# Kernel tuning notes

Measured on AMD Instinct MI355X. Metric: run time of the kernel, lower is better.

Reference implementation:

```python
import jax, jax.numpy as jnp
import numpy as np

N_NODES = 50000
N_EDGES = 600000
CH = 128


def _mlp(h, w1, b1, w2, b2):
    # Linear -> ReLU -> Linear (weights stored [in, out])
    return jax.nn.relu(h @ w1 + b1) @ w2 + b2


def setup_inputs() -> dict:
    key = jax.random.key(0)
    ks = jax.random.split(key, 12)
    def lin(k, fan_in, fan_out):
        bound = 1.0 / np.sqrt(fan_in)
        kw, kb = jax.random.split(k)
        w = jax.random.uniform(kw, (fan_in, fan_out), jnp.float32, -bound, bound)
        b = jax.random.uniform(kb, (fan_out,), jnp.float32, -bound, bound)
        return w, b
    ew1, eb1 = lin(ks[0], 3 * CH, CH)
    ew2, eb2 = lin(ks[1], CH, CH)
    nw1, nb1 = lin(ks[2], 2 * CH, CH)
    nw2, nb2 = lin(ks[3], CH, CH)
    x = jax.random.normal(ks[4], (N_NODES, CH), jnp.float32)
    edge_attr = jax.random.normal(ks[5], (N_EDGES, CH), jnp.float32)
    edge_index = jax.random.randint(ks[6], (2, N_EDGES), 0, N_NODES, jnp.int64 if jax.config.read('jax_enable_x64') else jnp.int32)
    return {"x": x, "edge_index": edge_index, "edge_attr": edge_attr,
            "ew1": ew1, "eb1": eb1, "ew2": ew2, "eb2": eb2,
            "nw1": nw1, "nb1": nb1, "nw2": nw2, "nb2": nb2}


def reference(x, edge_index, edge_attr, ew1, eb1, ew2, eb2, nw1, nb1, nw2, nb2):
    row, col = edge_index[0], edge_index[1]
    n = x.shape[0]
    # edge model: concat(source, target, edge_attr) -> MLP -> new edge_attr
    e_in = jnp.concatenate([x[row], x[col], edge_attr], axis=1)  # [E, 3*ch]
    new_edge_attr = _mlp(e_in, ew1, eb1, ew2, eb2)               # [E, ch]
    # node model: concat(x[col], new_edge_attr) -> MLP -> scatter_mean over row
    n_in = jnp.concatenate([x[col], new_edge_attr], axis=1)      # [E, 2*ch]
    msg = _mlp(n_in, nw1, nb1, nw2, nb2)                         # [E, ch]
    seg_sum = jax.ops.segment_sum(msg, row, num_segments=n)      # [N, ch]
    cnt = jax.ops.segment_sum(jnp.ones((msg.shape[0],), msg.dtype), row, num_segments=n)
    new_x = seg_sum / jnp.maximum(cnt, 1.0)[:, None]             # scatter_mean
    return new_x, new_edge_attr
```

## Files before the change

### kernel.cpp

```cpp
#include <hip/hip_runtime.h>
#include <stdint.h>

#define NN 50000
#define NE 600000
#define CH 128
#define RT 2
#define EPB 128

typedef __attribute__((ext_vector_type(8))) short short8;
typedef __attribute__((ext_vector_type(4))) float f32x4;
typedef __attribute__((ext_vector_type(4))) uint32_t u32x4;

__device__ __forceinline__ ushort f2bf(float f) {
  union { float f; uint32_t u; } v; v.f = f;
  uint32_t u = v.u;
  return (ushort)((u + 0x7FFFu + ((u >> 16) & 1u)) >> 16);
}
__device__ __forceinline__ float bf2f(uint32_t u16) {
  union { uint32_t u; float f; } t; t.u = u16 << 16; return t.f;
}
__device__ __forceinline__ uint32_t cvtpk_bf16(float a, float b) {
  uint32_t r;
  asm("v_cvt_pk_bf16_f32 %0, %1, %2" : "=v"(r) : "v"(a), "v"(b));
  return r;
}

__global__ void prep_frag_k(const float* __restrict__ ew1, const float* __restrict__ ew2,
                            const float* __restrict__ nw1, const float* __restrict__ nw2,
                            ushort* __restrict__ wB) {
  int idx = blockIdx.x * 256 + threadIdx.x;
  if (idx >= 114688) return;
  const float* src; int local;
  if (idx < 49152)      { src = ew1; local = idx; }
  else if (idx < 65536) { src = ew2; local = idx - 49152; }
  else if (idx < 98304) { src = nw1; local = idx - 65536; }
  else                  { src = nw2; local = idx - 98304; }
  int ks   = local >> 12;
  int rem  = local & 4095;
  int nt   = rem >> 9;
  int t    = rem & 511;
  int lane = t >> 3, i = t & 7;
  int k = ks * 32 + (lane >> 4) * 8 + i;
  int n = nt * 16 + (lane & 15);
  wB[idx] = f2bf(src[k * 128 + n]);
}

__global__ void convert_x_k(const float* __restrict__ x, ushort* __restrict__ xb) {
  int i = blockIdx.x * 256 + threadIdx.x;
  if (i >= NN * CH / 4) return;
  const float4 f = reinterpret_cast<const float4*>(x)[i];
  ushort4 r;
  r.x = f2bf(f.x); r.y = f2bf(f.y); r.z = f2bf(f.z); r.w = f2bf(f.w);
  reinterpret_cast<ushort4*>(xb)[i] = r;
}

__global__ void rank_k(const int* __restrict__ ei, unsigned* __restrict__ cnt,
                       unsigned* __restrict__ rank) {
  int e = blockIdx.x * 256 + threadIdx.x;
  if (e < NE) rank[e] = atomicAdd(&cnt[ei[e]], 1u);
}

__global__ void scan_k(const unsigned* __restrict__ cnt, unsigned* __restrict__ start) {
  __shared__ unsigned s[1024];
  const int CHUNK = (NN + 1023) / 1024;
  int t = threadIdx.x;
  int lo = t * CHUNK, hi = lo + CHUNK < NN ? lo + CHUNK : NN;
  unsigned sum = 0;
  for (int i = lo; i < hi; ++i) sum += cnt[i];
  s[t] = sum;
  __syncthreads();
  for (int off = 1; off < 1024; off <<= 1) {
    unsigned v = (t >= off) ? s[t - off] : 0u;
    __syncthreads();
    s[t] += v;
    __syncthreads();
  }
  unsigned run = t ? s[t - 1] : 0u;
  for (int i = lo; i < hi; ++i) { start[i] = run; run += cnt[i]; }
}

__global__ void dest_k(const int* __restrict__ ei, const unsigned* __restrict__ start,
                       const unsigned* __restrict__ rank, unsigned* __restrict__ dest) {
  int e = blockIdx.x * 256 + threadIdx.x;
  if (e < NE) dest[e] = start[ei[e]] + rank[e];
}

__device__ __forceinline__ void mm8(const ushort* Bcbuf, int lane,
                                    const short8 a[RT], f32x4 acc[RT][8]) {
#pragma unroll
  for (int nt = 0; nt < 8; ++nt) {
    short8 b = *reinterpret_cast<const short8*>(Bcbuf + nt * 512 + lane * 8);
#pragma unroll
    for (int rt = 0; rt < RT; ++rt)
      acc[rt][nt] = __builtin_amdgcn_mfma_f32_16x16x32_bf16(a[rt], b, acc[rt][nt], 0, 0, 0);
  }
}

__global__ __launch_bounds__(256, 2) void fused_k(
    const int* __restrict__ ei, const float* __restrict__ edge_attr,
    const ushort* __restrict__ wB,
    const float* __restrict__ eb1, const float* __restrict__ eb2,
    const float* __restrict__ nb1, const float* __restrict__ nb2,
    const ushort* __restrict__ xb, const unsigned* __restrict__ dest,
    ushort* __restrict__ msg, float* __restrict__ out_e)
{
  __shared__ ushort hbuf[4][RT * 16][136];
  __shared__ ushort Bc[4][4096];
  const int tid  = threadIdx.x;
  const int lane = tid & 63;
  const int widx = tid >> 6;
  const int wbase = blockIdx.x * EPB + widx * (RT * 16);
  const int l15 = lane & 15;
  const int g = lane >> 4;
  const int kg = g * 8;
  ushort (*h)[136] = hbuf[widx];

  short8 bt[2][4];

#define LDB2(set, ph) do { \
    const ushort* _s = wB + (size_t)(ph) * 4096 + tid * 16; \
    bt[set][0] = *reinterpret_cast<const short8*>(_s); \
    bt[set][1] = *reinterpret_cast<const short8*>(_s + 8); \
    bt[set][2] = *reinterpret_cast<const short8*>(_s + 4096); \
    bt[set][3] = *reinterpret_cast<const short8*>(_s + 4096 + 8); \
  } while (0)
#define STB2(set, ph) do { \
    ushort* _d0 = &Bc[(ph) & 3][tid * 16]; \
    ushort* _d1 = &Bc[((ph) + 1) & 3][tid * 16]; \
    *reinterpret_cast<short8*>(_d0)     = bt[set][0]; \
    *reinterpret_cast<short8*>(_d0 + 8) = bt[set][1]; \
    *reinterpret_cast<short8*>(_d1)     = bt[set][2]; \
    *reinterpret_cast<short8*>(_d1 + 8) = bt[set][3]; \
  } while (0)
#define BAR() do { \
    asm volatile("s_waitcnt lgkmcnt(0)" ::: "memory"); \
    __builtin_amdgcn_s_barrier(); \
  } while (0)
#define STEP(s, A0, A1, DO_LDB, DO_STB, DO_BAR) do { \
    __builtin_amdgcn_s_setprio(1); \
    mm8(Bc[(2 * (s)) & 3], lane, A0, acc); \
    mm8(Bc[(2 * (s) + 1) & 3], lane, A1, acc); \
    __builtin_amdgcn_s_setprio(0); \
    if (DO_LDB) LDB2((s) & 1, 2 * (s) + 4); \
    if (DO_STB) STB2(((s) + 1) & 1, 2 * (s) + 2); \
    if (DO_BAR) BAR(); \
  } while (0)
#define LDH(dst, ksl) do { \
    _Pragma("unroll") \
    for (int _rt = 0; _rt < RT; ++_rt) \
      dst[_rt] = *reinterpret_cast<const short8*>(&h[_rt * 16 + l15][(ksl) * 32 + kg]); \
  } while (0)

  LDB2(0, 0);
  LDB2(1, 2);

  int rowA[RT], colA[RT], eAc[RT];
#pragma unroll
  for (int rt = 0; rt < RT; ++rt) {
    int e = wbase + rt * 16 + l15;
    eAc[rt] = e < NE ? e : NE - 1;
    rowA[rt] = ei[eAc[rt]];
    colA[rt] = ei[NE + eAc[rt]];
  }
  short8 axr[4][RT], axc[4][RT];
#pragma unroll
  for (int ksl = 0; ksl < 4; ++ksl)
#pragma unroll
    for (int rt = 0; rt < RT; ++rt) {
      axr[ksl][rt] = *reinterpret_cast<const short8*>(xb + rowA[rt] * CH + ksl * 32 + kg);
      axc[ksl][rt] = *reinterpret_cast<const short8*>(xb + colA[rt] * CH + ksl * 32 + kg);
    }
  short8 eab[4][RT];
#pragma unroll
  for (int ksl = 0; ksl < 4; ++ksl)
#pragma unroll
    for (int rt = 0; rt < RT; ++rt) {
      const float* pp = edge_attr + (size_t)eAc[rt] * CH + ksl * 32 + kg;
      float4 f0 = *reinterpret_cast<const float4*>(pp);
      float4 f1 = *reinterpret_cast<const float4*>(pp + 4);
      union { u32x4 u; short8 s; } cv;
      cv.u = (u32x4){ cvtpk_bf16(f0.x, f0.y), cvtpk_bf16(f0.z, f0.w),
                      cvtpk_bf16(f1.x, f1.y), cvtpk_bf16(f1.z, f1.w) };
      eab[ksl][rt] = cv.s;
    }
  unsigned dp[RT * 4];
#pragma unroll
  for (int it = 0; it < RT * 4; ++it) {
    int er = wbase + it * 4 + g;
    dp[it] = dest[er < NE ? er : NE - 1];
  }

  STB2(0, 0);
  BAR();

  const f32x4 zero4 = {0.f, 0.f, 0.f, 0.f};
  f32x4 acc[RT][8];
  short8 ha0[RT], ha1[RT];

#pragma unroll
  for (int rt = 0; rt < RT; ++rt)
#pragma unroll
    for (int nt = 0; nt < 8; ++nt) acc[rt][nt] = zero4;

  STEP(0, axr[0], axr[1], 1, 1, 1);
  STEP(1, axr[2], axr[3], 1, 1, 1);
  STEP(2, axc[0], axc[1], 1, 1, 1);
  STEP(3, axc[2], axc[3], 1, 1, 1);
  STEP(4, eab[0], eab[1], 1, 1, 1);
  STEP(5, eab[2], eab[3], 1, 1, 1);
#pragma unroll
  for (int nt = 0; nt < 8; ++nt) {
    float bb = eb1[nt * 16 + l15];
#pragma unroll
    for (int rt = 0; rt < RT; ++rt)
#pragma unroll
      for (int r = 0; r < 4; r += 2) {
        float v0 = fmaxf(acc[rt][nt][r] + bb, 0.f);
        float v1 = fmaxf(acc[rt][nt][r + 1] + bb, 0.f);
        uint32_t pk = cvtpk_bf16(v0, v1);
        h[rt * 16 + g * 4 + r][nt * 16 + l15]     = (ushort)(pk & 0xffffu);
        h[rt * 16 + g * 4 + r + 1][nt * 16 + l15] = (ushort)(pk >> 16);
      }
  }

#pragma unroll
  for (int rt = 0; rt < RT; ++rt)
#pragma unroll
    for (int nt = 0; nt < 8; ++nt) acc[rt][nt] = zero4;
  LDH(ha0, 0); LDH(ha1, 1);
  STEP(6, ha0, ha1, 1, 1, 1);
  LDH(ha0, 2); LDH(ha1, 3);
  STEP(7, ha0, ha1, 1, 1, 1);
#pragma unroll
  for (int nt = 0; nt < 8; ++nt) {
    float bb = eb2[nt * 16 + l15];
#pragma unroll
    for (int rt = 0; rt < RT; ++rt) {
      float v[4];
#pragma unroll
      for (int r = 0; r < 4; ++r) {
        v[r] = acc[rt][nt][r] + bb;
        int erow = wbase + rt * 16 + g * 4 + r;
        if (erow < NE) out_e[(size_t)erow * CH + nt * 16 + l15] = v[r];
      }
#pragma unroll
      for (int r = 0; r < 4; r += 2) {
        uint32_t pk = cvtpk_bf16(v[r], v[r + 1]);
        h[rt * 16 + g * 4 + r][nt * 16 + l15]     = (ushort)(pk & 0xffffu);
        h[rt * 16 + g * 4 + r + 1][nt * 16 + l15] = (ushort)(pk >> 16);
      }
    }
  }

#pragma unroll
  for (int rt = 0; rt < RT; ++rt)
#pragma unroll
    for (int nt = 0; nt < 8; ++nt) acc[rt][nt] = zero4;
  STEP(8, axc[0], axc[1], 1, 1, 1);
  STEP(9, axc[2], axc[3], 1, 1, 1);
  LDH(ha0, 0); LDH(ha1, 1);
  STEP(10, ha0, ha1, 1, 1, 1);
  LDH(ha0, 2); LDH(ha1, 3);
  STEP(11, ha0, ha1, 1, 1, 1);
#pragma unroll
  for (int nt = 0; nt < 8; ++nt) {
    float bb = nb1[nt * 16 + l15];
#pragma unroll
    for (int rt = 0; rt < RT; ++rt)
#pragma unroll
      for (int r = 0; r < 4; r += 2) {
        float v0 = fmaxf(acc[rt][nt][r] + bb, 0.f);
        float v1 = fmaxf(acc[rt][nt][r + 1] + bb, 0.f);
        uint32_t pk = cvtpk_bf16(v0, v1);
        h[rt * 16 + g * 4 + r][nt * 16 + l15]     = (ushort)(pk & 0xffffu);
        h[rt * 16 + g * 4 + r + 1][nt * 16 + l15] = (ushort)(pk >> 16);
      }
  }

#pragma unroll
  for (int rt = 0; rt < RT; ++rt)
#pragma unroll
    for (int nt = 0; nt < 8; ++nt) acc[rt][nt] = zero4;
  LDH(ha0, 0); LDH(ha1, 1);
  STEP(12, ha0, ha1, 0, 1, 1);
  LDH(ha0, 2); LDH(ha1, 3);
  STEP(13, ha0, ha1, 0, 0, 0);
#pragma unroll
  for (int nt = 0; nt < 8; ++nt) {
    float bb = nb2[nt * 16 + l15];
#pragma unroll
    for (int rt = 0; rt < RT; ++rt)
#pragma unroll
      for (int r = 0; r < 4; r += 2) {
        uint32_t pk = cvtpk_bf16(acc[rt][nt][r] + bb, acc[rt][nt][r + 1] + bb);
        h[rt * 16 + g * 4 + r][nt * 16 + l15]     = (ushort)(pk & 0xffffu);
        h[rt * 16 + g * 4 + r + 1][nt * 16 + l15] = (ushort)(pk >> 16);
      }
  }
#pragma unroll
  for (int it = 0; it < RT * 4; ++it) {
    int row = it * 4 + g;
    int er = wbase + row;
    int col = l15 * 8;
    short8 v = *reinterpret_cast<const short8*>(&h[row][col]);
    if (er < NE)
      *reinterpret_cast<short8*>(msg + (size_t)dp[it] * CH + col) = v;
  }
#undef LDB2
#undef STB2
#undef BAR
#undef STEP
#undef LDH
}

__global__ __launch_bounds__(256) void reduce_k(const ushort* __restrict__ msg,
    const unsigned* __restrict__ cnt, const unsigned* __restrict__ start,
    float* __restrict__ out_x) {
  int w = blockIdx.x * 4 + (threadIdx.x >> 6);
  if (w >= NN) return;
  int lane = threadIdx.x & 63;
  unsigned deg = cnt[w], s = start[w];
  float a0 = 0.f, a1 = 0.f;
#pragma unroll 4
  for (unsigned j = 0; j < deg; ++j) {
    uint32_t pk = *reinterpret_cast<const uint32_t*>(msg + (size_t)(s + j) * CH + lane * 2);
    a0 += bf2f(pk & 0xffffu);
    a1 += bf2f(pk >> 16);
  }
  float inv = 1.0f / fmaxf((float)deg, 1.0f);
  float2 o; o.x = a0 * inv; o.y = a1 * inv;
  *reinterpret_cast<float2*>(out_x + (size_t)w * CH + lane * 2) = o;
}

extern "C" void kernel_launch(void* const* d_in, const int* in_sizes, int n_in,
                              void* d_out, int out_size, void* d_ws, size_t ws_size,
                              hipStream_t stream) {
  const float* x   = (const float*)d_in[0];
  const int*   ei  = (const int*)d_in[1];
  const float* ea  = (const float*)d_in[2];
  const float* ew1 = (const float*)d_in[3];
  const float* eb1 = (const float*)d_in[4];
  const float* ew2 = (const float*)d_in[5];
  const float* eb2 = (const float*)d_in[6];
  const float* nw1 = (const float*)d_in[7];
  const float* nb1 = (const float*)d_in[8];
  const float* nw2 = (const float*)d_in[9];
  const float* nb2 = (const float*)d_in[10];

  float* out_x = (float*)d_out;
  float* out_e = (float*)d_out + (size_t)NN * CH;

  char* wsb = (char*)d_ws;
  ushort*   msg    = (ushort*)wsb;
  ushort*   wB     = (ushort*)(wsb + 153600000);
  ushort*   xb     = (ushort*)(wsb + 153829376);
  unsigned* cnt    = (unsigned*)(wsb + 166629376);
  unsigned* start  = (unsigned*)(wsb + 166829376);
  unsigned* rank   = (unsigned*)(wsb + 167029376);
  unsigned* dest   = (unsigned*)(wsb + 169429376);

  hipMemsetAsync(cnt, 0, (size_t)NN * sizeof(unsigned), stream);

  prep_frag_k<<<448, 256, 0, stream>>>(ew1, ew2, nw1, nw2, wB);
  convert_x_k<<<(NN * CH / 4 + 255) / 256, 256, 0, stream>>>(x, xb);
  rank_k<<<(NE + 255) / 256, 256, 0, stream>>>(ei, cnt, rank);
  scan_k<<<1, 1024, 0, stream>>>(cnt, start);
  dest_k<<<(NE + 255) / 256, 256, 0, stream>>>(ei, start, rank, dest);

  int nblk = (NE + EPB - 1) / EPB;
  fused_k<<<nblk, 256, 0, stream>>>(ei, ea, wB, eb1, eb2, nb1, nb2, xb, dest, msg, out_e);

  reduce_k<<<(NN + 3) / 4, 256, 0, stream>>>(msg, cnt, start, out_x);
}
```

Measured before the change: 434.7 us.

## Enlarge per-wave edge tile, swizzle LDS hidden buffer, merge prep kernels

Raises the number of 16-row tiles per wave from 2 to 3, so each block covers 192 edges and every loaded weight fragment feeds more MFMAs. Replaces the padded LDS hidden-state array with an XOR-swizzled layout to avoid bank conflicts without padding. Merges the three independent preprocessing kernels into one launch to cut launch overhead. The extra accumulators raise register pressure, which may lower occupancy under the launch bound of two blocks.

New measurement: 535.9 us. +23.3%, slower.

```diff
diff --git a/kernel.cpp b/kernel.cpp
--- a/kernel.cpp
+++ b/kernel.cpp
@@ -4,8 +4,8 @@
 #define NN 50000
 #define NE 600000
 #define CH 128
-#define RT 2
-#define EPB 128
+#define RT 3
+#define EPB 192
 
 typedef __attribute__((ext_vector_type(8))) short short8;
 typedef __attribute__((ext_vector_type(4))) float f32x4;
@@ -25,39 +25,38 @@
   return r;
 }
 
-__global__ void prep_frag_k(const float* __restrict__ ew1, const float* __restrict__ ew2,
-                            const float* __restrict__ nw1, const float* __restrict__ nw2,
-                            ushort* __restrict__ wB) {
-  int idx = blockIdx.x * 256 + threadIdx.x;
-  if (idx >= 114688) return;
-  const float* src; int local;
-  if (idx < 49152)      { src = ew1; local = idx; }
-  else if (idx < 65536) { src = ew2; local = idx - 49152; }
-  else if (idx < 98304) { src = nw1; local = idx - 65536; }
-  else                  { src = nw2; local = idx - 98304; }
-  int ks   = local >> 12;
-  int rem  = local & 4095;
-  int nt   = rem >> 9;
-  int t    = rem & 511;
-  int lane = t >> 3, i = t & 7;
-  int k = ks * 32 + (lane >> 4) * 8 + i;
-  int n = nt * 16 + (lane & 15);
-  wB[idx] = f2bf(src[k * 128 + n]);
-}
-
-__global__ void convert_x_k(const float* __restrict__ x, ushort* __restrict__ xb) {
-  int i = blockIdx.x * 256 + threadIdx.x;
-  if (i >= NN * CH / 4) return;
-  const float4 f = reinterpret_cast<const float4*>(x)[i];
-  ushort4 r;
-  r.x = f2bf(f.x); r.y = f2bf(f.y); r.z = f2bf(f.z); r.w = f2bf(f.w);
-  reinterpret_cast<ushort4*>(xb)[i] = r;
-}
-
-__global__ void rank_k(const int* __restrict__ ei, unsigned* __restrict__ cnt,
-                       unsigned* __restrict__ rank) {
-  int e = blockIdx.x * 256 + threadIdx.x;
-  if (e < NE) rank[e] = atomicAdd(&cnt[ei[e]], 1u);
+__global__ void prep_all_k(const float* __restrict__ ew1, const float* __restrict__ ew2,
+                           const float* __restrict__ nw1, const float* __restrict__ nw2,
+                           ushort* __restrict__ wB,
+                           const float* __restrict__ x, ushort* __restrict__ xb,
+                           const int* __restrict__ ei, unsigned* __restrict__ cnt,
+                           unsigned* __restrict__ rank) {
+  int b = blockIdx.x, tid = threadIdx.x;
+  if (b < 448) {
+    int idx = b * 256 + tid;
+    const float* src; int local;
+    if (idx < 49152)      { src = ew1; local = idx; }
+    else if (idx < 65536) { src = ew2; local = idx - 49152; }
+    else if (idx < 98304) { src = nw1; local = idx - 65536; }
+    else                  { src = nw2; local = idx - 98304; }
+    int ks   = local >> 12;
+    int rem  = local & 4095;
+    int nt   = rem >> 9;
+    int t    = rem & 511;
+    int lane = t >> 3, i = t & 7;
+    int k = ks * 32 + (lane >> 4) * 8 + i;
+    int n = nt * 16 + (lane & 15);
+    wB[idx] = f2bf(src[k * 128 + n]);
+  } else if (b < 6698) {
+    int i = (b - 448) * 256 + tid;
+    const float4 f = reinterpret_cast<const float4*>(x)[i];
+    ushort4 r;
+    r.x = f2bf(f.x); r.y = f2bf(f.y); r.z = f2bf(f.z); r.w = f2bf(f.w);
+    reinterpret_cast<ushort4*>(xb)[i] = r;
+  } else {
+    int e = (b - 6698) * 256 + tid;
+    if (e < NE) rank[e] = atomicAdd(&cnt[ei[e]], 1u);
+  }
 }
 
 __global__ void scan_k(const unsigned* __restrict__ cnt, unsigned* __restrict__ start) {
@@ -85,6 +84,10 @@
   if (e < NE) dest[e] = start[ei[e]] + rank[e];
 }
 
+__device__ __forceinline__ ushort* hptr(ushort* hb, int row, int col) {
+  return (ushort*)((char*)hb + row * 256 + ((col * 2) ^ ((row & 7) << 4)));
+}
+
 __device__ __forceinline__ void mm8(const ushort* Bcbuf, int lane,
                                     const short8 a[RT], f32x4 acc[RT][8]) {
 #pragma unroll
@@ -104,7 +107,7 @@
     const ushort* __restrict__ xb, const unsigned* __restrict__ dest,
     ushort* __restrict__ msg, float* __restrict__ out_e)
 {
-  __shared__ ushort hbuf[4][RT * 16][136];
+  __shared__ ushort hbuf[4][RT * 16 * 128];
   __shared__ ushort Bc[4][4096];
   const int tid  = threadIdx.x;
   const int lane = tid & 63;
@@ -113,7 +116,7 @@
   const int l15 = lane & 15;
   const int g = lane >> 4;
   const int kg = g * 8;
-  ushort (*h)[136] = hbuf[widx];
+  ushort* hb = hbuf[widx];
 
   short8 bt[2][4];
 
@@ -148,7 +151,7 @@
 #define LDH(dst, ksl) do { \
     _Pragma("unroll") \
     for (int _rt = 0; _rt < RT; ++_rt) \
-      dst[_rt] = *reinterpret_cast<const short8*>(&h[_rt * 16 + l15][(ksl) * 32 + kg]); \
+      dst[_rt] = *reinterpret_cast<const short8*>(hptr(hb, _rt * 16 + l15, (ksl) * 32 + kg)); \
   } while (0)
 
   LDB2(0, 0);
@@ -218,8 +221,8 @@
         float v0 = fmaxf(acc[rt][nt][r] + bb, 0.f);
         float v1 = fmaxf(acc[rt][nt][r + 1] + bb, 0.f);
         uint32_t pk = cvtpk_bf16(v0, v1);
-        h[rt * 16 + g * 4 + r][nt * 16 + l15]     = (ushort)(pk & 0xffffu);
-        h[rt * 16 + g * 4 + r + 1][nt * 16 + l15] = (ushort)(pk >> 16);
+        *hptr(hb, rt * 16 + g * 4 + r,     nt * 16 + l15) = (ushort)(pk & 0xffffu);
+        *hptr(hb, rt * 16 + g * 4 + r + 1, nt * 16 + l15) = (ushort)(pk >> 16);
       }
   }
 
@@ -246,8 +249,8 @@
 #pragma unroll
       for (int r = 0; r < 4; r += 2) {
         uint32_t pk = cvtpk_bf16(v[r], v[r + 1]);
-        h[rt * 16 + g * 4 + r][nt * 16 + l15]     = (ushort)(pk & 0xffffu);
-        h[rt * 16 + g * 4 + r + 1][nt * 16 + l15] = (ushort)(pk >> 16);
+        *hptr(hb, rt * 16 + g * 4 + r,     nt * 16 + l15) = (ushort)(pk & 0xffffu);
+        *hptr(hb, rt * 16 + g * 4 + r + 1, nt * 16 + l15) = (ushort)(pk >> 16);
       }
     }
   }
@@ -272,8 +275,8 @@
         float v0 = fmaxf(acc[rt][nt][r] + bb, 0.f);
         float v1 = fmaxf(acc[rt][nt][r + 1] + bb, 0.f);
         uint32_t pk = cvtpk_bf16(v0, v1);
-        h[rt * 16 + g * 4 + r][nt * 16 + l15]     = (ushort)(pk & 0xffffu);
-        h[rt * 16 + g * 4 + r + 1][nt * 16 + l15] = (ushort)(pk >> 16);
+        *hptr(hb, rt * 16 + g * 4 + r,     nt * 16 + l15) = (ushort)(pk & 0xffffu);
+        *hptr(hb, rt * 16 + g * 4 + r + 1, nt * 16 + l15) = (ushort)(pk >> 16);
       }
   }
 
@@ -293,8 +296,8 @@
 #pragma unroll
       for (int r = 0; r < 4; r += 2) {
         uint32_t pk = cvtpk_bf16(acc[rt][nt][r] + bb, acc[rt][nt][r + 1] + bb);
-        h[rt * 16 + g * 4 + r][nt * 16 + l15]     = (ushort)(pk & 0xffffu);
-        h[rt * 16 + g * 4 + r + 1][nt * 16 + l15] = (ushort)(pk >> 16);
+        *hptr(hb, rt * 16 + g * 4 + r,     nt * 16 + l15) = (ushort)(pk & 0xffffu);
+        *hptr(hb, rt * 16 + g * 4 + r + 1, nt * 16 + l15) = (ushort)(pk >> 16);
       }
   }
 #pragma unroll
@@ -302,7 +305,7 @@
     int row = it * 4 + g;
     int er = wbase + row;
     int col = l15 * 8;
-    short8 v = *reinterpret_cast<const short8*>(&h[row][col]);
+    short8 v = *reinterpret_cast<const short8*>(hptr(hb, row, col));
     if (er < NE)
       *reinterpret_cast<short8*>(msg + (size_t)dp[it] * CH + col) = v;
   }
@@ -361,9 +364,7 @@
 
   hipMemsetAsync(cnt, 0, (size_t)NN * sizeof(unsigned), stream);
 
-  prep_frag_k<<<448, 256, 0, stream>>>(ew1, ew2, nw1, nw2, wB);
-  convert_x_k<<<(NN * CH / 4 + 255) / 256, 256, 0, stream>>>(x, xb);
-  rank_k<<<(NE + 255) / 256, 256, 0, stream>>>(ei, cnt, rank);
+  prep_all_k<<<9042, 256, 0, stream>>>(ew1, ew2, nw1, nw2, wB, x, xb, ei, cnt, rank);
   scan_k<<<1, 1024, 0, stream>>>(cnt, start);
   dest_k<<<(NE + 255) / 256, 256, 0, stream>>>(ei, start, rank, dest);
 
```
